# Performance work log

Measured on AMD Instinct MI355X. Metric: run time of the kernel, lower is better.

## Reference

```python
import jax, jax.numpy as jnp
import numpy as np


def setup_inputs() -> dict:
    key = jax.random.key(0)
    k1, k2 = jax.random.split(key)
    B, S, D, C = 4, 4096, 256, 8921
    x = jax.random.normal(k1, (B, S, D), dtype=jnp.float32)
    # nn.Linear(input_size, num_classes).weight has shape [C, D]
    W = jax.random.normal(k2, (C, D), dtype=jnp.float32) * (1.0 / np.sqrt(D))
    return {"x": x, "W": W}


def reference(x, W):
    # scores: Linear(x) -> [B, S, C], transpose(1,2) -> [B, C, S]
    scores = jnp.einsum("bsd,cd->bcs", x, W)
    attention = jax.nn.softmax(scores, axis=-1)          # [B, C, S]
    logits = jnp.einsum("bcs,bsd->bcd", attention, x)    # bmm -> [B, C, D]
    return (logits, attention)
```

## Files before the change

### kernel.cpp

```cpp
#include <hip/hip_runtime.h>
#include <hip/hip_bf16.h>

constexpr int Bn   = 4;
constexpr int Sn   = 4096;
constexpr int Dn   = 256;
constexpr int Cn   = 8921;
constexpr int Cpad = 8960;

typedef unsigned short u16;
typedef short v8s __attribute__((ext_vector_type(8)));
typedef float v4f __attribute__((ext_vector_type(4)));

constexpr size_t OFF_W  = 0;
constexpr size_t OFF_X  = OFF_W  + (size_t)Cpad * Dn * 2;
constexpr size_t OFF_XT = OFF_X  + (size_t)Bn * Sn * Dn * 2;
constexpr size_t OFF_L  = OFF_XT + (size_t)Bn * Sn * Dn * 2;
constexpr size_t OFF_E  = OFF_L  + (size_t)Bn * Cpad * 4;
constexpr size_t WS_NEED = OFF_E + (size_t)Bn * Cpad * Sn * 2;

__device__ __forceinline__ u16 f2bs(float x) { __bf16 b = (__bf16)x; return __builtin_bit_cast(u16, b); }
__device__ __forceinline__ float b2f(u16 u)  { return __uint_as_float(((unsigned)u) << 16); }

#define GLD16(g, l) __builtin_amdgcn_global_load_lds( \
    (const __attribute__((address_space(1))) unsigned int*)(g), \
    (__attribute__((address_space(3))) unsigned int*)(l), 16, 0, 0)

__global__ __launch_bounds__(256) void k_conv_w(const float* __restrict__ Wsrc,
                                                u16* __restrict__ Wb,
                                                float* __restrict__ lsum) {
    int idx = blockIdx.x * 256 + threadIdx.x;
    if (idx < (Cn * Dn) / 4) {
        float4 v = ((const float4*)Wsrc)[idx];
        ushort4 o; o.x = f2bs(v.x); o.y = f2bs(v.y); o.z = f2bs(v.z); o.w = f2bs(v.w);
        ((ushort4*)Wb)[idx] = o;
    }
    if (idx < Bn * Cpad) lsum[idx] = 0.f;
}

__global__ __launch_bounds__(256) void k_conv_x(const float* __restrict__ x,
                                                u16* __restrict__ xb,
                                                u16* __restrict__ xt) {
    __shared__ u16 tile[64][65];
    const int t  = threadIdx.x;
    const int b  = blockIdx.z;
    const int s0 = blockIdx.x * 64, d0 = blockIdx.y * 64;
    const float* xs = x + (size_t)b * Sn * Dn;
    u16* xbb = xb + (size_t)b * Sn * Dn;
    u16* xtb = xt + (size_t)b * Dn * Sn;
    const int rr = t >> 4, cc = (t & 15) * 4;
#pragma unroll
    for (int i = 0; i < 4; i++) {
        int srow = i * 16 + rr;
        float4 v = *(const float4*)(xs + (size_t)(s0 + srow) * Dn + d0 + cc);
        ushort4 o; o.x = f2bs(v.x); o.y = f2bs(v.y); o.z = f2bs(v.z); o.w = f2bs(v.w);
        *(ushort4*)(xbb + (size_t)(s0 + srow) * Dn + d0 + cc) = o;
        tile[srow][cc] = o.x; tile[srow][cc + 1] = o.y; tile[srow][cc + 2] = o.z; tile[srow][cc + 3] = o.w;
    }
    __syncthreads();
#pragma unroll
    for (int i = 0; i < 4; i++) {
        int drow = i * 16 + rr;
        ushort4 o;
        o.x = tile[cc][drow]; o.y = tile[cc + 1][drow]; o.z = tile[cc + 2][drow]; o.w = tile[cc + 3][drow];
        *(ushort4*)(xtb + (size_t)(d0 + drow) * Sn + s0 + cc) = o;
    }
}

__global__ __launch_bounds__(256) void k_qk(const u16* __restrict__ Wb,
                                            const u16* __restrict__ xb,
                                            u16* __restrict__ est,
                                            float* __restrict__ lsum) {
    __shared__ u16 sA[128 * 64];
    __shared__ u16 sB[128 * 64];
    const int t  = threadIdx.x;
    const int b  = blockIdx.z;
    const int c0 = blockIdx.y * 128;
    const int s0 = blockIdx.x * 128;
    const u16* xbb = xb + (size_t)b * Sn * Dn;
    const int w = t >> 6, l = t & 63;
    const int wm = w >> 1, wn = w & 1;
    const int lr = l & 15, lq = l >> 4;

    v4f acc[4][4] = {};

    for (int ks = 0; ks < 4; ++ks) {
        __syncthreads();
#pragma unroll
        for (int i = 0; i < 4; i++) {
            int q = i * 256 + t;
            int row = q >> 3, pc = q & 7;
            int lc = pc ^ (row & 7);
            int grow = c0 + row; if (grow >= Cn) grow = Cn - 1;
            GLD16(Wb  + (size_t)grow * Dn        + ks * 64 + lc * 8, (char*)sA + q * 16);
            GLD16(xbb + (size_t)(s0 + row) * Dn  + ks * 64 + lc * 8, (char*)sB + q * 16);
        }
        __syncthreads();
#pragma unroll
        for (int kc = 0; kc < 2; kc++) {
            v8s af[4], bfv[4];
#pragma unroll
            for (int mi = 0; mi < 4; mi++) {
                int row = wm * 64 + mi * 16 + lr;
                int pc = (kc * 4 + lq) ^ (row & 7);
                af[mi] = *(const v8s*)(sA + row * 64 + pc * 8);
            }
#pragma unroll
            for (int ni = 0; ni < 4; ni++) {
                int row = wn * 64 + ni * 16 + lr;
                int pc = (kc * 4 + lq) ^ (row & 7);
                bfv[ni] = *(const v8s*)(sB + row * 64 + pc * 8);
            }
#pragma unroll
            for (int mi = 0; mi < 4; mi++)
#pragma unroll
                for (int ni = 0; ni < 4; ni++)
                    acc[mi][ni] = __builtin_amdgcn_mfma_f32_16x16x32_bf16(af[mi], bfv[ni], acc[mi][ni], 0, 0, 0);
        }
    }

#pragma unroll
    for (int mi = 0; mi < 4; mi++)
#pragma unroll
        for (int ni = 0; ni < 4; ni++)
#pragma unroll
            for (int r = 0; r < 4; r++)
                acc[mi][ni][r] = __expf(acc[mi][ni][r]);

    float* lb = lsum + (size_t)b * Cpad;
#pragma unroll
    for (int mi = 0; mi < 4; mi++)
#pragma unroll
        for (int r = 0; r < 4; r++) {
            float s = acc[mi][0][r] + acc[mi][1][r] + acc[mi][2][r] + acc[mi][3][r];
            s += __shfl_xor(s, 1); s += __shfl_xor(s, 2); s += __shfl_xor(s, 4); s += __shfl_xor(s, 8);
            if (lr == 0) atomicAdd(lb + (c0 + wm * 64 + mi * 16 + lq * 4 + r), s);
        }

    u16* eb = est + (size_t)b * Cpad * Sn + (size_t)c0 * Sn + s0;
#pragma unroll
    for (int mi = 0; mi < 4; mi++)
#pragma unroll
        for (int ni = 0; ni < 4; ni++)
#pragma unroll
            for (int r = 0; r < 4; r++) {
                int row = wm * 64 + mi * 16 + lq * 4 + r;
                int col = wn * 64 + ni * 16 + lr;
                eb[(size_t)row * Sn + col] = f2bs(acc[mi][ni][r]);
            }
}

__global__ __launch_bounds__(256) void k_pv(const u16* __restrict__ est,
                                            const u16* __restrict__ xt,
                                            const float* __restrict__ lsum,
                                            float* __restrict__ out) {
    __shared__ u16 sA[64 * 64];
    __shared__ u16 sB[256 * 64];
    __shared__ float rinv[64];
    const int t  = threadIdx.x;
    const int b  = blockIdx.y;
    const int c0 = blockIdx.x * 64;
    const int w = t >> 6, l = t & 63;
    const int lr = l & 15, lq = l >> 4;
    const u16* eb  = est + (size_t)b * Cpad * Sn;
    const u16* xtb = xt  + (size_t)b * Dn * Sn;
    float* attn = out + (size_t)Bn * Cn * Dn + (size_t)b * Cn * Sn;

    if (t < 64) rinv[t] = 1.f / lsum[(size_t)b * Cpad + c0 + t];

    v4f acc[4][4] = {};

    for (int ks = 0; ks < 64; ++ks) {
        __syncthreads();
#pragma unroll
        for (int i = 0; i < 2; i++) {
            int q = i * 256 + t; int row = q >> 3, pc = q & 7, lc = pc ^ (row & 7);
            GLD16(eb + (size_t)(c0 + row) * Sn + ks * 64 + lc * 8, (char*)sA + q * 16);
        }
#pragma unroll
        for (int i = 0; i < 8; i++) {
            int q = i * 256 + t; int row = q >> 3, pc = q & 7, lc = pc ^ (row & 7);
            GLD16(xtb + (size_t)row * Sn + ks * 64 + lc * 8, (char*)sB + q * 16);
        }
        __syncthreads();

#pragma unroll
        for (int i = 0; i < 2; i++) {
            int q = i * 256 + t; int row = q >> 3, pc = q & 7, lc = pc ^ (row & 7);
            int c = c0 + row;
            if (c < Cn) {
                v8s v = *(const v8s*)(sA + q * 8);
                float rv = rinv[row];
                float4 o0, o1;
                o0.x = b2f((u16)v[0]) * rv; o0.y = b2f((u16)v[1]) * rv;
                o0.z = b2f((u16)v[2]) * rv; o0.w = b2f((u16)v[3]) * rv;
                o1.x = b2f((u16)v[4]) * rv; o1.y = b2f((u16)v[5]) * rv;
                o1.z = b2f((u16)v[6]) * rv; o1.w = b2f((u16)v[7]) * rv;
                float* dst = attn + (size_t)c * Sn + ks * 64 + lc * 8;
                *(float4*)dst = o0;
                *(float4*)(dst + 4) = o1;
            }
        }

#pragma unroll
        for (int kc = 0; kc < 2; kc++) {
            v8s af[4], bfv[4];
#pragma unroll
            for (int mi = 0; mi < 4; mi++) {
                int row = mi * 16 + lr;
                int pc = (kc * 4 + lq) ^ (row & 7);
                af[mi] = *(const v8s*)(sA + row * 64 + pc * 8);
            }
#pragma unroll
            for (int ni = 0; ni < 4; ni++) {
                int row = w * 64 + ni * 16 + lr;
                int pc = (kc * 4 + lq) ^ (row & 7);
                bfv[ni] = *(const v8s*)(sB + row * 64 + pc * 8);
            }
#pragma unroll
            for (int mi = 0; mi < 4; mi++)
#pragma unroll
                for (int ni = 0; ni < 4; ni++)
                    acc[mi][ni] = __builtin_amdgcn_mfma_f32_16x16x32_bf16(af[mi], bfv[ni], acc[mi][ni], 0, 0, 0);
        }
    }

#pragma unroll
    for (int mi = 0; mi < 4; mi++)
#pragma unroll
        for (int r = 0; r < 4; r++) {
            int row = mi * 16 + lq * 4 + r;
            int c = c0 + row;
            if (c < Cn) {
                float rv = rinv[row];
#pragma unroll
                for (int ni = 0; ni < 4; ni++) {
                    int col = w * 64 + ni * 16 + lr;
                    out[((size_t)b * Cn + c) * Dn + col] = acc[mi][ni][r] * rv;
                }
            }
        }
}

extern "C" void kernel_launch(void* const* d_in, const int* in_sizes, int n_in,
                              void* d_out, int out_size, void* d_ws, size_t ws_size,
                              hipStream_t stream) {
    const float* x = (const float*)d_in[0];
    const float* W = (const float*)d_in[1];
    float* out = (float*)d_out;
    if (ws_size < WS_NEED) return;

    char* ws = (char*)d_ws;
    u16*   Wb = (u16*)(ws + OFF_W);
    u16*   xb = (u16*)(ws + OFF_X);
    u16*   xt = (u16*)(ws + OFF_XT);
    float* ls = (float*)(ws + OFF_L);
    u16*   es = (u16*)(ws + OFF_E);

    k_conv_w<<<(570944 + 255) / 256, 256, 0, stream>>>(W, Wb, ls);
    k_conv_x<<<dim3(Sn / 64, Dn / 64, Bn), 256, 0, stream>>>(x, xb, xt);
    k_qk<<<dim3(Sn / 128, Cpad / 128, Bn), 256, 0, stream>>>(Wb, xb, es, ls);
    k_pv<<<dim3(Cpad / 64, Bn), 256, 0, stream>>>(es, xt, ls, out);
}
```

Baseline: 1.015 ms.

## Fuse QK, softmax and PV into one two-pass kernel recomputing scores

Replaces the separate score and PV kernels with a single kernel per 160-class block. It first computes the row sums of exp(scores) over all of S, then recomputes the scores to write normalized attention and feed the exp values through LDS into the PV MFMA. The bf16 exp intermediate in global memory (about 290MB written and read) goes away, along with the global atomics. In exchange the QK GEMM is done twice and only 56x4 workgroups are launched, which may leave the GPU underoccupied.

```diff
diff --git a/kernel.cpp b/kernel.cpp
--- a/kernel.cpp
+++ b/kernel.cpp
@@ -1,40 +1,37 @@
 #include <hip/hip_runtime.h>
 #include <hip/hip_bf16.h>
 
-constexpr int Bn   = 4;
-constexpr int Sn   = 4096;
-constexpr int Dn   = 256;
-constexpr int Cn   = 8921;
-constexpr int Cpad = 8960;
+constexpr int Bn = 4;
+constexpr int Sn = 4096;
+constexpr int Dn = 256;
+constexpr int Cn = 8921;
+constexpr int BM = 160;
+constexpr int NCB = 56;
+constexpr int NIT = Sn / 128;
 
 typedef unsigned short u16;
 typedef short v8s __attribute__((ext_vector_type(8)));
 typedef float v4f __attribute__((ext_vector_type(4)));
 
 constexpr size_t OFF_W  = 0;
-constexpr size_t OFF_X  = OFF_W  + (size_t)Cpad * Dn * 2;
+constexpr size_t OFF_X  = OFF_W  + (size_t)8960 * Dn * 2;
 constexpr size_t OFF_XT = OFF_X  + (size_t)Bn * Sn * Dn * 2;
-constexpr size_t OFF_L  = OFF_XT + (size_t)Bn * Sn * Dn * 2;
-constexpr size_t OFF_E  = OFF_L  + (size_t)Bn * Cpad * 4;
-constexpr size_t WS_NEED = OFF_E + (size_t)Bn * Cpad * Sn * 2;
+constexpr size_t WS_NEED = OFF_XT + (size_t)Bn * Sn * Dn * 2;
 
 __device__ __forceinline__ u16 f2bs(float x) { __bf16 b = (__bf16)x; return __builtin_bit_cast(u16, b); }
-__device__ __forceinline__ float b2f(u16 u)  { return __uint_as_float(((unsigned)u) << 16); }
-
-#define GLD16(g, l) __builtin_amdgcn_global_load_lds( \
-    (const __attribute__((address_space(1))) unsigned int*)(g), \
-    (__attribute__((address_space(3))) unsigned int*)(l), 16, 0, 0)
+
+#define GLD16(g_, l_) __builtin_amdgcn_global_load_lds( \
+    (const __attribute__((address_space(1))) unsigned int*)(g_), \
+    (__attribute__((address_space(3))) unsigned int*)(l_), 16, 0, 0)
 
 __global__ __launch_bounds__(256) void k_conv_w(const float* __restrict__ Wsrc,
-                                                u16* __restrict__ Wb,
-                                                float* __restrict__ lsum) {
+                                                u16* __restrict__ Wb) {
     int idx = blockIdx.x * 256 + threadIdx.x;
     if (idx < (Cn * Dn) / 4) {
         float4 v = ((const float4*)Wsrc)[idx];
         ushort4 o; o.x = f2bs(v.x); o.y = f2bs(v.y); o.z = f2bs(v.z); o.w = f2bs(v.w);
         ((ushort4*)Wb)[idx] = o;
     }
-    if (idx < Bn * Cpad) lsum[idx] = 0.f;
 }
 
 __global__ __launch_bounds__(256) void k_conv_x(const float* __restrict__ x,
@@ -66,176 +63,210 @@
     }
 }
 
-__global__ __launch_bounds__(256) void k_qk(const u16* __restrict__ Wb,
-                                            const u16* __restrict__ xb,
-                                            u16* __restrict__ est,
-                                            float* __restrict__ lsum) {
-    __shared__ u16 sA[128 * 64];
-    __shared__ u16 sB[128 * 64];
+constexpr int L_XB0 = 0;
+constexpr int L_XB1 = 16384;
+constexpr int L_WB0 = 32768;
+constexpr int L_WB1 = 53248;
+constexpr int L_E   = 73728;
+constexpr int L_L   = 114688;
+constexpr int L_TOT = 114688 + 640;
+
+__device__ __forceinline__ void stage_xb(const u16* xbb, char* lds, int t, int it, int ks, int buf) {
+#pragma unroll
+    for (int i = 0; i < 2; i++) {
+        int q = i * 512 + t;
+        int row = q >> 3, oct = q & 7, lc = oct ^ (row & 7);
+        GLD16(xbb + (size_t)(it * 128 + row) * Dn + ks * 64 + lc * 8,
+              lds + (buf ? L_XB1 : L_XB0) + q * 16);
+    }
+}
+
+__device__ __forceinline__ void stage_wb(const u16* Wb, char* lds, int t, int c0, int ks, int buf) {
+#pragma unroll
+    for (int i = 0; i < 3; i++) {
+        int q = i * 512 + t;
+        if (q < 1280) {
+            int row = q >> 3, oct = q & 7, lc = oct ^ (row & 7);
+            int grow = c0 + row; if (grow >= Cn) grow = Cn - 1;
+            GLD16(Wb + (size_t)grow * Dn + ks * 64 + lc * 8,
+                  lds + (buf ? L_WB1 : L_WB0) + q * 16);
+        }
+    }
+}
+
+__device__ __forceinline__ void qk_it(const u16* Wb, const u16* xbb, char* lds,
+                                      int t, int c0, int it, v4f (&acc)[5][2]) {
+    const int l  = t & 63, w = t >> 6;
+    const int wm = w >> 2, wn = w & 3;
+    const int lr = l & 15, lq = l >> 4;
+    stage_xb(xbb, lds, t, it, 0, 0);
+    stage_wb(Wb, lds, t, c0, 0, 0);
+    __syncthreads();
+#pragma unroll
+    for (int ks = 0; ks < 4; ks++) {
+        if (ks < 3) {
+            stage_xb(xbb, lds, t, it, ks + 1, (ks + 1) & 1);
+            stage_wb(Wb, lds, t, c0, ks + 1, (ks + 1) & 1);
+        }
+        const u16* A  = (const u16*)(lds + ((ks & 1) ? L_WB1 : L_WB0));
+        const u16* Bx = (const u16*)(lds + ((ks & 1) ? L_XB1 : L_XB0));
+#pragma unroll
+        for (int kc = 0; kc < 2; kc++) {
+            v8s af[5], bf[2];
+#pragma unroll
+            for (int mi = 0; mi < 5; mi++) {
+                int row = wm * 80 + mi * 16 + lr;
+                int oct = (kc * 4 + lq) ^ (row & 7);
+                af[mi] = *(const v8s*)(A + row * 64 + oct * 8);
+            }
+#pragma unroll
+            for (int ni = 0; ni < 2; ni++) {
+                int row = wn * 32 + ni * 16 + lr;
+                int oct = (kc * 4 + lq) ^ (row & 7);
+                bf[ni] = *(const v8s*)(Bx + row * 64 + oct * 8);
+            }
+#pragma unroll
+            for (int mi = 0; mi < 5; mi++)
+#pragma unroll
+                for (int ni = 0; ni < 2; ni++)
+                    acc[mi][ni] = __builtin_amdgcn_mfma_f32_16x16x32_bf16(af[mi], bf[ni], acc[mi][ni], 0, 0, 0);
+        }
+        __syncthreads();
+    }
+}
+
+__global__ __launch_bounds__(512, 2) void k_main(const u16* __restrict__ Wb,
+                                                 const u16* __restrict__ xb,
+                                                 const u16* __restrict__ xt,
+                                                 float* __restrict__ out) {
+    __shared__ __align__(16) char lds[L_TOT];
     const int t  = threadIdx.x;
-    const int b  = blockIdx.z;
-    const int c0 = blockIdx.y * 128;
-    const int s0 = blockIdx.x * 128;
+    const int c0 = blockIdx.x * BM;
+    const int b  = blockIdx.y;
     const u16* xbb = xb + (size_t)b * Sn * Dn;
-    const int w = t >> 6, l = t & 63;
-    const int wm = w >> 1, wn = w & 1;
+    const u16* xtb = xt + (size_t)b * Dn * Sn;
+    const int l  = t & 63, w = t >> 6;
+    const int wm = w >> 2, wn = w & 3;
     const int lr = l & 15, lq = l >> 4;
-
-    v4f acc[4][4] = {};
-
-    for (int ks = 0; ks < 4; ++ks) {
+    float* lbuf = (float*)(lds + L_L);
+    if (t < BM) lbuf[t] = 0.f;
+
+#pragma unroll 1
+    for (int it = 0; it < NIT; ++it) {
+        v4f acc[5][2] = {};
+        qk_it(Wb, xbb, lds, t, c0, it, acc);
+#pragma unroll
+        for (int mi = 0; mi < 5; mi++)
+#pragma unroll
+            for (int r = 0; r < 4; r++) {
+                float s = __expf(acc[mi][0][r]) + __expf(acc[mi][1][r]);
+                s += __shfl_xor(s, 1); s += __shfl_xor(s, 2);
+                s += __shfl_xor(s, 4); s += __shfl_xor(s, 8);
+                if (lr == 0) atomicAdd(&lbuf[wm * 80 + mi * 16 + lq * 4 + r], s);
+            }
+    }
+    __syncthreads();
+    if (t < BM) lbuf[t] = 1.f / lbuf[t];
+    __syncthreads();
+    float rv[5][4];
+#pragma unroll
+    for (int mi = 0; mi < 5; mi++)
+#pragma unroll
+        for (int r = 0; r < 4; r++)
+            rv[mi][r] = lbuf[wm * 80 + mi * 16 + lq * 4 + r];
+
+    float* attn = out + (size_t)Bn * Cn * Dn + (size_t)b * Cn * Sn;
+    u16* sE = (u16*)(lds + L_E);
+    v4f accp[5][4] = {};
+
+#pragma unroll 1
+    for (int it = 0; it < NIT; ++it) {
+        v4f acc[5][2] = {};
+        qk_it(Wb, xbb, lds, t, c0, it, acc);
+
+#pragma unroll
+        for (int i = 0; i < 4; i++) {
+            int q = i * 512 + t;
+            int row = q >> 3, oct = q & 7, lc = oct ^ (row & 7);
+            GLD16(xtb + (size_t)row * Sn + it * 128 + lc * 8, lds + q * 16);
+        }
+#pragma unroll
+        for (int mi = 0; mi < 5; mi++)
+#pragma unroll
+            for (int ni = 0; ni < 2; ni++)
+#pragma unroll
+                for (int r = 0; r < 4; r++) {
+                    float e = __expf(acc[mi][ni][r]);
+                    acc[mi][ni][r] = e;
+                    int rloc = lq * 4 + r;
+                    int row = wm * 80 + mi * 16 + rloc;
+                    int col = wn * 32 + ni * 16 + lr;
+                    int oct = (col >> 3) ^ rloc;
+                    sE[row * 128 + oct * 8 + (lr & 7)] = f2bs(e);
+                }
+#pragma unroll
+        for (int mi = 0; mi < 5; mi++)
+#pragma unroll
+            for (int r = 0; r < 4; r++) {
+                int c = c0 + wm * 80 + mi * 16 + lq * 4 + r;
+                if (c < Cn) {
+                    float rvv = rv[mi][r];
+#pragma unroll
+                    for (int ni = 0; ni < 2; ni++) {
+                        int s = it * 128 + wn * 32 + ni * 16 + lr;
+                        attn[(size_t)c * Sn + s] = acc[mi][ni][r] * rvv;
+                    }
+                }
+            }
         __syncthreads();
-#pragma unroll
-        for (int i = 0; i < 4; i++) {
-            int q = i * 256 + t;
-            int row = q >> 3, pc = q & 7;
-            int lc = pc ^ (row & 7);
-            int grow = c0 + row; if (grow >= Cn) grow = Cn - 1;
-            GLD16(Wb  + (size_t)grow * Dn        + ks * 64 + lc * 8, (char*)sA + q * 16);
-            GLD16(xbb + (size_t)(s0 + row) * Dn  + ks * 64 + lc * 8, (char*)sB + q * 16);
-        }
-        __syncthreads();
-#pragma unroll
-        for (int kc = 0; kc < 2; kc++) {
-            v8s af[4], bfv[4];
-#pragma unroll
-            for (int mi = 0; mi < 4; mi++) {
-                int row = wm * 64 + mi * 16 + lr;
-                int pc = (kc * 4 + lq) ^ (row & 7);
-                af[mi] = *(const v8s*)(sA + row * 64 + pc * 8);
-            }
-#pragma unroll
-            for (int ni = 0; ni < 4; ni++) {
-                int row = wn * 64 + ni * 16 + lr;
-                int pc = (kc * 4 + lq) ^ (row & 7);
-                bfv[ni] = *(const v8s*)(sB + row * 64 + pc * 8);
-            }
-#pragma unroll
-            for (int mi = 0; mi < 4; mi++)
-#pragma unroll
-                for (int ni = 0; ni < 4; ni++)
-                    acc[mi][ni] = __builtin_amdgcn_mfma_f32_16x16x32_bf16(af[mi], bfv[ni], acc[mi][ni], 0, 0, 0);
-        }
-    }
-
-#pragma unroll
-    for (int mi = 0; mi < 4; mi++)
-#pragma unroll
-        for (int ni = 0; ni < 4; ni++)
-#pragma unroll
-            for (int r = 0; r < 4; r++)
-                acc[mi][ni][r] = __expf(acc[mi][ni][r]);
-
-    float* lb = lsum + (size_t)b * Cpad;
-#pragma unroll
-    for (int mi = 0; mi < 4; mi++)
+
+#pragma unroll
+        for (int ks2 = 0; ks2 < 2; ks2++) {
+            if (ks2 == 0) {
+#pragma unroll
+                for (int i = 0; i < 4; i++) {
+                    int q = i * 512 + t;
+                    int row = q >> 3, oct = q & 7, lc = oct ^ (row & 7);
+                    GLD16(xtb + (size_t)row * Sn + it * 128 + 64 + lc * 8, lds + 32768 + q * 16);
+                }
+            }
+            const u16* X = (const u16*)(lds + (ks2 ? 32768 : 0));
+#pragma unroll
+            for (int kc = 0; kc < 2; kc++) {
+                v8s ae[5], bt[4];
+#pragma unroll
+                for (int mi = 0; mi < 5; mi++) {
+                    int row = wm * 80 + mi * 16 + lr;
+                    int oct = ((ks2 * 2 + kc) * 4 + lq) ^ lr;
+                    ae[mi] = *(const v8s*)(sE + row * 128 + oct * 8);
+                }
+#pragma unroll
+                for (int ni = 0; ni < 4; ni++) {
+                    int row = wn * 64 + ni * 16 + lr;
+                    int oct = (kc * 4 + lq) ^ (row & 7);
+                    bt[ni] = *(const v8s*)(X + row * 64 + oct * 8);
+                }
+#pragma unroll
+                for (int mi = 0; mi < 5; mi++)
+#pragma unroll
+                    for (int ni = 0; ni < 4; ni++)
+                        accp[mi][ni] = __builtin_amdgcn_mfma_f32_16x16x32_bf16(ae[mi], bt[ni], accp[mi][ni], 0, 0, 0);
+            }
+            __syncthreads();
+        }
+    }
+
+#pragma unroll
+    for (int mi = 0; mi < 5; mi++)
 #pragma unroll
         for (int r = 0; r < 4; r++) {
-            float s = acc[mi][0][r] + acc[mi][1][r] + acc[mi][2][r] + acc[mi][3][r];
-            s += __shfl_xor(s, 1); s += __shfl_xor(s, 2); s += __shfl_xor(s, 4); s += __shfl_xor(s, 8);
-            if (lr == 0) atomicAdd(lb + (c0 + wm * 64 + mi * 16 + lq * 4 + r), s);
-        }
-
-    u16* eb = est + (size_t)b * Cpad * Sn + (size_t)c0 * Sn + s0;
-#pragma unroll
-    for (int mi = 0; mi < 4; mi++)
-#pragma unroll
-        for (int ni = 0; ni < 4; ni++)
-#pragma unroll
-            for (int r = 0; r < 4; r++) {
-                int row = wm * 64 + mi * 16 + lq * 4 + r;
-                int col = wn * 64 + ni * 16 + lr;
-                eb[(size_t)row * Sn + col] = f2bs(acc[mi][ni][r]);
-            }
-}
-
-__global__ __launch_bounds__(256) void k_pv(const u16* __restrict__ est,
-                                            const u16* __restrict__ xt,
-                                            const float* __restrict__ lsum,
-                                            float* __restrict__ out) {
-    __shared__ u16 sA[64 * 64];
-    __shared__ u16 sB[256 * 64];
-    __shared__ float rinv[64];
-    const int t  = threadIdx.x;
-    const int b  = blockIdx.y;
-    const int c0 = blockIdx.x * 64;
-    const int w = t >> 6, l = t & 63;
-    const int lr = l & 15, lq = l >> 4;
-    const u16* eb  = est + (size_t)b * Cpad * Sn;
-    const u16* xtb = xt  + (size_t)b * Dn * Sn;
-    float* attn = out + (size_t)Bn * Cn * Dn + (size_t)b * Cn * Sn;
-
-    if (t < 64) rinv[t] = 1.f / lsum[(size_t)b * Cpad + c0 + t];
-
-    v4f acc[4][4] = {};
-
-    for (int ks = 0; ks < 64; ++ks) {
-        __syncthreads();
-#pragma unroll
-        for (int i = 0; i < 2; i++) {
-            int q = i * 256 + t; int row = q >> 3, pc = q & 7, lc = pc ^ (row & 7);
-            GLD16(eb + (size_t)(c0 + row) * Sn + ks * 64 + lc * 8, (char*)sA + q * 16);
-        }
-#pragma unroll
-        for (int i = 0; i < 8; i++) {
-            int q = i * 256 + t; int row = q >> 3, pc = q & 7, lc = pc ^ (row & 7);
-            GLD16(xtb + (size_t)row * Sn + ks * 64 + lc * 8, (char*)sB + q * 16);
-        }
-        __syncthreads();
-
-#pragma unroll
-        for (int i = 0; i < 2; i++) {
-            int q = i * 256 + t; int row = q >> 3, pc = q & 7, lc = pc ^ (row & 7);
-            int c = c0 + row;
+            int c = c0 + wm * 80 + mi * 16 + lq * 4 + r;
             if (c < Cn) {
-                v8s v = *(const v8s*)(sA + q * 8);
-                float rv = rinv[row];
-                float4 o0, o1;
-                o0.x = b2f((u16)v[0]) * rv; o0.y = b2f((u16)v[1]) * rv;
-                o0.z = b2f((u16)v[2]) * rv; o0.w = b2f((u16)v[3]) * rv;
-                o1.x = b2f((u16)v[4]) * rv; o1.y = b2f((u16)v[5]) * rv;
-                o1.z = b2f((u16)v[6]) * rv; o1.w = b2f((u16)v[7]) * rv;
-                float* dst = attn + (size_t)c * Sn + ks * 64 + lc * 8;
-                *(float4*)dst = o0;
-                *(float4*)(dst + 4) = o1;
-            }
-        }
-
-#pragma unroll
-        for (int kc = 0; kc < 2; kc++) {
-            v8s af[4], bfv[4];
-#pragma unroll
-            for (int mi = 0; mi < 4; mi++) {
-                int row = mi * 16 + lr;
-                int pc = (kc * 4 + lq) ^ (row & 7);
-                af[mi] = *(const v8s*)(sA + row * 64 + pc * 8);
-            }
-#pragma unroll
-            for (int ni = 0; ni < 4; ni++) {
-                int row = w * 64 + ni * 16 + lr;
-                int pc = (kc * 4 + lq) ^ (row & 7);
-                bfv[ni] = *(const v8s*)(sB + row * 64 + pc * 8);
-            }
-#pragma unroll
-            for (int mi = 0; mi < 4; mi++)
-#pragma unroll
-                for (int ni = 0; ni < 4; ni++)
-                    acc[mi][ni] = __builtin_amdgcn_mfma_f32_16x16x32_bf16(af[mi], bfv[ni], acc[mi][ni], 0, 0, 0);
-        }
-    }
-
-#pragma unroll
-    for (int mi = 0; mi < 4; mi++)
-#pragma unroll
-        for (int r = 0; r < 4; r++) {
-            int row = mi * 16 + lq * 4 + r;
-            int c = c0 + row;
-            if (c < Cn) {
-                float rv = rinv[row];
+                float rvv = rv[mi][r];
 #pragma unroll
                 for (int ni = 0; ni < 4; ni++) {
-                    int col = w * 64 + ni * 16 + lr;
-                    out[((size_t)b * Cn + c) * Dn + col] = acc[mi][ni][r] * rv;
+                    int d = wn * 64 + ni * 16 + lr;
+                    out[((size_t)b * Cn + c) * Dn + d] = accp[mi][ni][r] * rvv;
                 }
             }
         }
@@ -250,14 +281,11 @@
     if (ws_size < WS_NEED) return;
 
     char* ws = (char*)d_ws;
-    u16*   Wb = (u16*)(ws + OFF_W);
-    u16*   xb = (u16*)(ws + OFF_X);
-    u16*   xt = (u16*)(ws + OFF_XT);
-    float* ls = (float*)(ws + OFF_L);
-    u16*   es = (u16*)(ws + OFF_E);
-
-    k_conv_w<<<(570944 + 255) / 256, 256, 0, stream>>>(W, Wb, ls);
+    u16* Wb = (u16*)(ws + OFF_W);
+    u16* xb = (u16*)(ws + OFF_X);
+    u16* xt = (u16*)(ws + OFF_XT);
+
+    k_conv_w<<<(Cn * Dn / 4 + 255) / 256, 256, 0, stream>>>(W, Wb);
     k_conv_x<<<dim3(Sn / 64, Dn / 64, Bn), 256, 0, stream>>>(x, xb, xt);
-    k_qk<<<dim3(Sn / 128, Cpad / 128, Bn), 256, 0, stream>>>(Wb, xb, es, ls);
-    k_pv<<<dim3(Cpad / 64, Bn), 256, 0, stream>>>(es, xt, ls, out);
-}
+    k_main<<<dim3(NCB, Bn), 512, 0, stream>>>(Wb, xb, xt, out);
+}
```

Measured after the change: 1.246 ms. 1.23x slower.

## Fuse QK, exp and PV into one flash-style kernel with separate normalize pass

Applied to the files above, without the earlier changes.

Replaces the separate QK-exp and PV kernels with one fused kernel per (batch, 64-class block). It computes exp(scores) for 128-position tiles into LDS, accumulates row sums in LDS, feeds the exponentials straight into the PV MFMA, and double-buffers the x/W/xT staging. The unnormalized exponentials are still written to workspace, and a new k_scale kernel then writes the normalized fp32 attention. This drops the PV kernel's re-read of the exponentials and the global atomics, at the cost of one extra kernel launch and a heavier LDS footprint per block.

```diff
diff --git a/kernel.cpp b/kernel.cpp
--- a/kernel.cpp
+++ b/kernel.cpp
@@ -6,6 +6,9 @@
 constexpr int Dn   = 256;
 constexpr int Cn   = 8921;
 constexpr int Cpad = 8960;
+constexpr int BM   = 64;
+constexpr int NCB  = 140;
+constexpr int NIT  = 32;
 
 typedef unsigned short u16;
 typedef short v8s __attribute__((ext_vector_type(8)));
@@ -21,20 +24,18 @@
 __device__ __forceinline__ u16 f2bs(float x) { __bf16 b = (__bf16)x; return __builtin_bit_cast(u16, b); }
 __device__ __forceinline__ float b2f(u16 u)  { return __uint_as_float(((unsigned)u) << 16); }
 
-#define GLD16(g, l) __builtin_amdgcn_global_load_lds( \
-    (const __attribute__((address_space(1))) unsigned int*)(g), \
-    (__attribute__((address_space(3))) unsigned int*)(l), 16, 0, 0)
+#define GLD16(g_, l_) __builtin_amdgcn_global_load_lds( \
+    (const __attribute__((address_space(1))) unsigned int*)(g_), \
+    (__attribute__((address_space(3))) unsigned int*)(l_), 16, 0, 0)
 
 __global__ __launch_bounds__(256) void k_conv_w(const float* __restrict__ Wsrc,
-                                                u16* __restrict__ Wb,
-                                                float* __restrict__ lsum) {
+                                                u16* __restrict__ Wb) {
     int idx = blockIdx.x * 256 + threadIdx.x;
     if (idx < (Cn * Dn) / 4) {
         float4 v = ((const float4*)Wsrc)[idx];
         ushort4 o; o.x = f2bs(v.x); o.y = f2bs(v.y); o.z = f2bs(v.z); o.w = f2bs(v.w);
         ((ushort4*)Wb)[idx] = o;
     }
-    if (idx < Bn * Cpad) lsum[idx] = 0.f;
 }
 
 __global__ __launch_bounds__(256) void k_conv_x(const float* __restrict__ x,
@@ -66,179 +67,186 @@
     }
 }
 
-__global__ __launch_bounds__(256) void k_qk(const u16* __restrict__ Wb,
-                                            const u16* __restrict__ xb,
-                                            u16* __restrict__ est,
-                                            float* __restrict__ lsum) {
-    __shared__ u16 sA[128 * 64];
-    __shared__ u16 sB[128 * 64];
-    const int t  = threadIdx.x;
-    const int b  = blockIdx.z;
-    const int c0 = blockIdx.y * 128;
-    const int s0 = blockIdx.x * 128;
+constexpr int L_WB = 32768;
+constexpr int L_E  = 49152;
+constexpr int L_LB = 65536;
+constexpr int L_TOT = 65792;
+
+__global__ __launch_bounds__(512, 4) void k_main(const u16* __restrict__ Wb,
+                                                 const u16* __restrict__ xb,
+                                                 const u16* __restrict__ xt,
+                                                 u16* __restrict__ est,
+                                                 float* __restrict__ lsum,
+                                                 float* __restrict__ out) {
+    __shared__ __align__(16) char lds[L_TOT];
+    const int bid = blockIdx.x;
+    const int nid = (bid & 7) * 70 + (bid >> 3);
+    const int b = nid / NCB, cblk = nid % NCB;
+    const int c0 = cblk * BM;
+
+    const int t = threadIdx.x;
+    const int w = t >> 6, l = t & 63;
+    const int lr = l & 15, lq = l >> 4;
+    const int wm = w >> 2, wn = w & 3;
     const u16* xbb = xb + (size_t)b * Sn * Dn;
-    const int w = t >> 6, l = t & 63;
-    const int wm = w >> 1, wn = w & 1;
-    const int lr = l & 15, lq = l >> 4;
-
-    v4f acc[4][4] = {};
-
-    for (int ks = 0; ks < 4; ++ks) {
+    const u16* xtb = xt + (size_t)b * Dn * Sn;
+    u16* sE = (u16*)(lds + L_E);
+    float* lbuf = (float*)(lds + L_LB);
+    u16* estash = est + (size_t)b * Cpad * Sn + (size_t)c0 * Sn;
+
+    auto stage_xb = [&](int it, int ks, int buf) {
+#pragma unroll
+        for (int i = 0; i < 2; i++) {
+            int q = i * 512 + t;
+            int row = q >> 3, pc = q & 7, lc = pc ^ (row & 7);
+            GLD16(xbb + (size_t)(it * 128 + row) * Dn + ks * 64 + lc * 8, lds + buf * 16384 + q * 16);
+        }
+    };
+    auto stage_wb = [&](int ks, int buf) {
+        int row = t >> 3, pc = t & 7, lc = pc ^ (row & 7);
+        int grow = c0 + row; if (grow >= Cn) grow = Cn - 1;
+        GLD16(Wb + (size_t)grow * Dn + ks * 64 + lc * 8, lds + L_WB + buf * 8192 + t * 16);
+    };
+    auto stage_xt = [&](int it, int q4, int buf) {
+#pragma unroll
+        for (int i = 0; i < 2; i++) {
+            int q = i * 512 + t;
+            int row = q >> 2, c2 = q & 3, lc = c2 ^ (row & 3);
+            GLD16(xtb + (size_t)row * Sn + it * 128 + q4 * 32 + lc * 8, lds + buf * 16384 + q * 16);
+        }
+    };
+
+    v4f accp[2][4] = {};
+
+    if (t < BM) lbuf[t] = 0.f;
+    stage_xb(0, 0, 0); stage_wb(0, 0);
+    __syncthreads();
+
+#pragma unroll 1
+    for (int it = 0; it < NIT; ++it) {
+        v4f acc[2][2] = {};
+#pragma unroll
+        for (int ks = 0; ks < 4; ks++) {
+            if (ks < 3) { stage_xb(it, ks + 1, (ks + 1) & 1); stage_wb(ks + 1, (ks + 1) & 1); }
+            const u16* A  = (const u16*)(lds + L_WB + (ks & 1) * 8192);
+            const u16* Bx = (const u16*)(lds + (ks & 1) * 16384);
+#pragma unroll
+            for (int kc = 0; kc < 2; kc++) {
+                v8s af[2], bf[2];
+#pragma unroll
+                for (int mi = 0; mi < 2; mi++) {
+                    int row = wm * 32 + mi * 16 + lr;
+                    int oct = (kc * 4 + lq) ^ (row & 7);
+                    af[mi] = *(const v8s*)(A + row * 64 + oct * 8);
+                }
+#pragma unroll
+                for (int ni = 0; ni < 2; ni++) {
+                    int row = wn * 32 + ni * 16 + lr;
+                    int oct = (kc * 4 + lq) ^ (row & 7);
+                    bf[ni] = *(const v8s*)(Bx + row * 64 + oct * 8);
+                }
+#pragma unroll
+                for (int mi = 0; mi < 2; mi++)
+#pragma unroll
+                    for (int ni = 0; ni < 2; ni++)
+                        acc[mi][ni] = __builtin_amdgcn_mfma_f32_16x16x32_bf16(af[mi], bf[ni], acc[mi][ni], 0, 0, 0);
+            }
+            __syncthreads();
+        }
+
+        stage_xt(it, 0, 0); stage_xt(it, 1, 1);
+#pragma unroll
+        for (int mi = 0; mi < 2; mi++)
+#pragma unroll
+            for (int r = 0; r < 4; r++) {
+                float e0 = __expf(acc[mi][0][r]);
+                float e1 = __expf(acc[mi][1][r]);
+                int rloc = lq * 4 + r;
+                int row = wm * 32 + mi * 16 + rloc;
+                int col0 = wn * 32 + lr;
+                int col1 = wn * 32 + 16 + lr;
+                sE[row * 128 + ((col0 >> 3) ^ rloc) * 8 + (lr & 7)] = f2bs(e0);
+                sE[row * 128 + ((col1 >> 3) ^ rloc) * 8 + (lr & 7)] = f2bs(e1);
+                float s = e0 + e1;
+                s += __shfl_xor(s, 1); s += __shfl_xor(s, 2);
+                s += __shfl_xor(s, 4); s += __shfl_xor(s, 8);
+                if (lr == 0) atomicAdd(&lbuf[row], s);
+            }
         __syncthreads();
-#pragma unroll
-        for (int i = 0; i < 4; i++) {
-            int q = i * 256 + t;
-            int row = q >> 3, pc = q & 7;
-            int lc = pc ^ (row & 7);
-            int grow = c0 + row; if (grow >= Cn) grow = Cn - 1;
-            GLD16(Wb  + (size_t)grow * Dn        + ks * 64 + lc * 8, (char*)sA + q * 16);
-            GLD16(xbb + (size_t)(s0 + row) * Dn  + ks * 64 + lc * 8, (char*)sB + q * 16);
-        }
-        __syncthreads();
-#pragma unroll
-        for (int kc = 0; kc < 2; kc++) {
-            v8s af[4], bfv[4];
-#pragma unroll
-            for (int mi = 0; mi < 4; mi++) {
-                int row = wm * 64 + mi * 16 + lr;
-                int pc = (kc * 4 + lq) ^ (row & 7);
-                af[mi] = *(const v8s*)(sA + row * 64 + pc * 8);
+
+#pragma unroll
+        for (int i = 0; i < 2; i++) {
+            int q = i * 512 + t;
+            int row = q >> 4, oc = q & 15, oa = oc ^ (row & 15);
+            v8s v = *(const v8s*)(sE + row * 128 + oa * 8);
+            *(v8s*)(estash + (size_t)row * Sn + it * 128 + oc * 8) = v;
+        }
+
+#pragma unroll
+        for (int q4 = 0; q4 < 4; q4++) {
+            const u16* X = (const u16*)(lds + (q4 & 1) * 16384);
+            v8s ae[2], bt[4];
+#pragma unroll
+            for (int mi = 0; mi < 2; mi++) {
+                int row = wm * 32 + mi * 16 + lr;
+                int oct = (q4 * 4 + lq) ^ lr;
+                ae[mi] = *(const v8s*)(sE + row * 128 + oct * 8);
             }
 #pragma unroll
             for (int ni = 0; ni < 4; ni++) {
                 int row = wn * 64 + ni * 16 + lr;
-                int pc = (kc * 4 + lq) ^ (row & 7);
-                bfv[ni] = *(const v8s*)(sB + row * 64 + pc * 8);
-            }
-#pragma unroll
-            for (int mi = 0; mi < 4; mi++)
+                int o4 = lq ^ (row & 3);
+                bt[ni] = *(const v8s*)(X + row * 32 + o4 * 8);
+            }
+#pragma unroll
+            for (int mi = 0; mi < 2; mi++)
 #pragma unroll
                 for (int ni = 0; ni < 4; ni++)
-                    acc[mi][ni] = __builtin_amdgcn_mfma_f32_16x16x32_bf16(af[mi], bfv[ni], acc[mi][ni], 0, 0, 0);
-        }
-    }
-
-#pragma unroll
-    for (int mi = 0; mi < 4; mi++)
-#pragma unroll
-        for (int ni = 0; ni < 4; ni++)
-#pragma unroll
-            for (int r = 0; r < 4; r++)
-                acc[mi][ni][r] = __expf(acc[mi][ni][r]);
-
-    float* lb = lsum + (size_t)b * Cpad;
-#pragma unroll
-    for (int mi = 0; mi < 4; mi++)
+                    accp[mi][ni] = __builtin_amdgcn_mfma_f32_16x16x32_bf16(ae[mi], bt[ni], accp[mi][ni], 0, 0, 0);
+            __syncthreads();
+            if (q4 < 2)      stage_xt(it, q4 + 2, q4 & 1);
+            else if (q4 == 2 && it + 1 < NIT) { stage_xb(it + 1, 0, 0); stage_wb(0, 0); }
+        }
+    }
+
+    float rv_[2][4];
+#pragma unroll
+    for (int mi = 0; mi < 2; mi++)
+#pragma unroll
+        for (int r = 0; r < 4; r++)
+            rv_[mi][r] = 1.f / lbuf[wm * 32 + mi * 16 + lq * 4 + r];
+#pragma unroll
+    for (int mi = 0; mi < 2; mi++)
 #pragma unroll
         for (int r = 0; r < 4; r++) {
-            float s = acc[mi][0][r] + acc[mi][1][r] + acc[mi][2][r] + acc[mi][3][r];
-            s += __shfl_xor(s, 1); s += __shfl_xor(s, 2); s += __shfl_xor(s, 4); s += __shfl_xor(s, 8);
-            if (lr == 0) atomicAdd(lb + (c0 + wm * 64 + mi * 16 + lq * 4 + r), s);
-        }
-
-    u16* eb = est + (size_t)b * Cpad * Sn + (size_t)c0 * Sn + s0;
-#pragma unroll
-    for (int mi = 0; mi < 4; mi++)
-#pragma unroll
-        for (int ni = 0; ni < 4; ni++)
-#pragma unroll
-            for (int r = 0; r < 4; r++) {
-                int row = wm * 64 + mi * 16 + lq * 4 + r;
-                int col = wn * 64 + ni * 16 + lr;
-                eb[(size_t)row * Sn + col] = f2bs(acc[mi][ni][r]);
-            }
-}
-
-__global__ __launch_bounds__(256) void k_pv(const u16* __restrict__ est,
-                                            const u16* __restrict__ xt,
-                                            const float* __restrict__ lsum,
-                                            float* __restrict__ out) {
-    __shared__ u16 sA[64 * 64];
-    __shared__ u16 sB[256 * 64];
-    __shared__ float rinv[64];
-    const int t  = threadIdx.x;
-    const int b  = blockIdx.y;
-    const int c0 = blockIdx.x * 64;
-    const int w = t >> 6, l = t & 63;
-    const int lr = l & 15, lq = l >> 4;
-    const u16* eb  = est + (size_t)b * Cpad * Sn;
-    const u16* xtb = xt  + (size_t)b * Dn * Sn;
-    float* attn = out + (size_t)Bn * Cn * Dn + (size_t)b * Cn * Sn;
-
-    if (t < 64) rinv[t] = 1.f / lsum[(size_t)b * Cpad + c0 + t];
-
-    v4f acc[4][4] = {};
-
-    for (int ks = 0; ks < 64; ++ks) {
-        __syncthreads();
-#pragma unroll
-        for (int i = 0; i < 2; i++) {
-            int q = i * 256 + t; int row = q >> 3, pc = q & 7, lc = pc ^ (row & 7);
-            GLD16(eb + (size_t)(c0 + row) * Sn + ks * 64 + lc * 8, (char*)sA + q * 16);
-        }
-#pragma unroll
-        for (int i = 0; i < 8; i++) {
-            int q = i * 256 + t; int row = q >> 3, pc = q & 7, lc = pc ^ (row & 7);
-            GLD16(xtb + (size_t)row * Sn + ks * 64 + lc * 8, (char*)sB + q * 16);
-        }
-        __syncthreads();
-
-#pragma unroll
-        for (int i = 0; i < 2; i++) {
-            int q = i * 256 + t; int row = q >> 3, pc = q & 7, lc = pc ^ (row & 7);
-            int c = c0 + row;
+            int c = c0 + wm * 32 + mi * 16 + lq * 4 + r;
             if (c < Cn) {
-                v8s v = *(const v8s*)(sA + q * 8);
-                float rv = rinv[row];
-                float4 o0, o1;
-                o0.x = b2f((u16)v[0]) * rv; o0.y = b2f((u16)v[1]) * rv;
-                o0.z = b2f((u16)v[2]) * rv; o0.w = b2f((u16)v[3]) * rv;
-                o1.x = b2f((u16)v[4]) * rv; o1.y = b2f((u16)v[5]) * rv;
-                o1.z = b2f((u16)v[6]) * rv; o1.w = b2f((u16)v[7]) * rv;
-                float* dst = attn + (size_t)c * Sn + ks * 64 + lc * 8;
-                *(float4*)dst = o0;
-                *(float4*)(dst + 4) = o1;
-            }
-        }
-
-#pragma unroll
-        for (int kc = 0; kc < 2; kc++) {
-            v8s af[4], bfv[4];
-#pragma unroll
-            for (int mi = 0; mi < 4; mi++) {
-                int row = mi * 16 + lr;
-                int pc = (kc * 4 + lq) ^ (row & 7);
-                af[mi] = *(const v8s*)(sA + row * 64 + pc * 8);
-            }
-#pragma unroll
-            for (int ni = 0; ni < 4; ni++) {
-                int row = w * 64 + ni * 16 + lr;
-                int pc = (kc * 4 + lq) ^ (row & 7);
-                bfv[ni] = *(const v8s*)(sB + row * 64 + pc * 8);
-            }
-#pragma unroll
-            for (int mi = 0; mi < 4; mi++)
-#pragma unroll
-                for (int ni = 0; ni < 4; ni++)
-                    acc[mi][ni] = __builtin_amdgcn_mfma_f32_16x16x32_bf16(af[mi], bfv[ni], acc[mi][ni], 0, 0, 0);
-        }
-    }
-
-#pragma unroll
-    for (int mi = 0; mi < 4; mi++)
-#pragma unroll
-        for (int r = 0; r < 4; r++) {
-            int row = mi * 16 + lq * 4 + r;
-            int c = c0 + row;
-            if (c < Cn) {
-                float rv = rinv[row];
 #pragma unroll
                 for (int ni = 0; ni < 4; ni++) {
-                    int col = w * 64 + ni * 16 + lr;
-                    out[((size_t)b * Cn + c) * Dn + col] = acc[mi][ni][r] * rv;
+                    int d = wn * 64 + ni * 16 + lr;
+                    out[((size_t)b * Cn + c) * Dn + d] = accp[mi][ni][r] * rv_[mi][r];
                 }
             }
         }
+    if (t < BM) lsum[(size_t)b * Cpad + c0 + t] = lbuf[t];
+}
+
+__global__ __launch_bounds__(512) void k_scale(const u16* __restrict__ est,
+                                               const float* __restrict__ lsum,
+                                               float* __restrict__ out) {
+    const int c = blockIdx.x, b = blockIdx.y;
+    const float rv = 1.f / lsum[(size_t)b * Cpad + c];
+    const u16* er = est + ((size_t)b * Cpad + c) * Sn;
+    float* ar = out + (size_t)Bn * Cn * Dn + ((size_t)b * Cn + c) * Sn;
+    const int s = threadIdx.x * 8;
+    v8s v = *(const v8s*)(er + s);
+    float4 o0, o1;
+    o0.x = b2f((u16)v[0]) * rv; o0.y = b2f((u16)v[1]) * rv;
+    o0.z = b2f((u16)v[2]) * rv; o0.w = b2f((u16)v[3]) * rv;
+    o1.x = b2f((u16)v[4]) * rv; o1.y = b2f((u16)v[5]) * rv;
+    o1.z = b2f((u16)v[6]) * rv; o1.w = b2f((u16)v[7]) * rv;
+    *(float4*)(ar + s) = o0;
+    *(float4*)(ar + s + 4) = o1;
 }
 
 extern "C" void kernel_launch(void* const* d_in, const int* in_sizes, int n_in,
@@ -256,8 +264,8 @@
     float* ls = (float*)(ws + OFF_L);
     u16*   es = (u16*)(ws + OFF_E);
 
-    k_conv_w<<<(570944 + 255) / 256, 256, 0, stream>>>(W, Wb, ls);
+    k_conv_w<<<(Cn * Dn / 4 + 255) / 256, 256, 0, stream>>>(W, Wb);
     k_conv_x<<<dim3(Sn / 64, Dn / 64, Bn), 256, 0, stream>>>(x, xb, xt);
-    k_qk<<<dim3(Sn / 128, Cpad / 128, Bn), 256, 0, stream>>>(Wb, xb, es, ls);
-    k_pv<<<dim3(Cpad / 64, Bn), 256, 0, stream>>>(es, xt, ls, out);
-}
+    k_main<<<dim3(NCB * Bn), 512, 0, stream>>>(Wb, xb, xt, es, ls, out);
+    k_scale<<<dim3(Cn, Bn), 512, 0, stream>>>(es, ls, out);
+}
```

After: 1.216 ms. 19.8% more time.
